# Kernel tuning notes

Measured on AMD Instinct MI355X. Metric: run time of the kernel, lower is better.

Reference implementation:

```python
import jax, jax.numpy as jnp
import numpy as np

NX = 1024
N_HEAD = 16
HEAD_DIM = NX // N_HEAD
MASKED_BIAS = -10000.0


def setup_inputs() -> dict:
    key = jax.random.key(0)
    k1, k2, k3 = jax.random.split(key, 3)
    hidden_states = jax.random.normal(k1, (2, 2048, NX), dtype=jnp.float32)
    # Conv1D weights: stored [in, out], y = x @ W + b (like torch addmm)
    c_attn_w = jax.random.normal(k2, (NX, 3 * NX), dtype=jnp.float32) * 0.02
    c_attn_b = jnp.zeros((3 * NX,), dtype=jnp.float32)
    c_proj_w = jax.random.normal(k3, (NX, NX), dtype=jnp.float32) * 0.02
    c_proj_b = jnp.zeros((NX,), dtype=jnp.float32)
    return {
        "hidden_states": hidden_states,
        "c_attn_w": c_attn_w,
        "c_attn_b": c_attn_b,
        "c_proj_w": c_proj_w,
        "c_proj_b": c_proj_b,
    }


def reference(hidden_states, c_attn_w, c_attn_b, c_proj_w, c_proj_b):
    B, S, _ = hidden_states.shape
    qkv = hidden_states @ c_attn_w + c_attn_b  # [B, S, 3*NX]
    q, k, v = jnp.split(qkv, 3, axis=-1)
    # split heads -> [B, H, S, D]
    def split_heads(x):
        return x.reshape(B, S, N_HEAD, HEAD_DIM).transpose(0, 2, 1, 3)
    q, k, v = split_heads(q), split_heads(k), split_heads(v)
    # scores scaled by sqrt(head_dim) (v.size(-1)**0.5 in original)
    w = jnp.einsum("bhqd,bhkd->bhqk", q, k) / jnp.sqrt(jnp.float32(HEAD_DIM))
    # causal mask (nd == ns here since no past)
    causal = jnp.tril(jnp.ones((S, S), dtype=bool))
    w = jnp.where(causal[None, None, :, :], w, jnp.float32(MASKED_BIAS))
    w = jax.nn.softmax(w, axis=-1)
    a = jnp.einsum("bhqk,bhkd->bhqd", w, v)  # [B, H, S, D]
    # merge heads
    a = a.transpose(0, 2, 1, 3).reshape(B, S, NX)
    out = a @ c_proj_w + c_proj_b
    return out
```

## Files before the change

kernel.cpp:

```cpp
#include <hip/hip_runtime.h>
#include <hip/hip_bf16.h>
#include <cmath>

typedef __attribute__((ext_vector_type(8))) short bf16x8;
typedef __attribute__((ext_vector_type(4))) float f32x4;

#define NXC 1024
#define NH 16
#define HD 64
#define BATCH 2
#define SEQ 2048
#define TOK (BATCH * SEQ)

__device__ __forceinline__ ushort f2bf(float f) {
  unsigned u;
  asm("v_cvt_pk_bf16_f32 %0, %1, %2" : "=v"(u) : "v"(f), "v"(f));
  return (ushort)u;
}

__device__ __forceinline__ void gload_lds16(const void* g, void* lds) {
  __builtin_amdgcn_global_load_lds(
      (const __attribute__((address_space(1))) void*)g,
      (__attribute__((address_space(3))) void*)lds, 16, 0, 0);
}

__device__ __forceinline__ float fast_exp2(float x) {
  float r;
  asm("v_exp_f32 %0, %1" : "=v"(r) : "v"(x));
  return r;
}

template <int CTRL>
__device__ __forceinline__ float dpp_mov(float x) {
  return __builtin_bit_cast(
      float, __builtin_amdgcn_mov_dpp(__builtin_bit_cast(int, x), CTRL, 0xF, 0xF, true));
}
__device__ __forceinline__ float red16_max(float x) {
  x = fmaxf(x, dpp_mov<0x121>(x));
  x = fmaxf(x, dpp_mov<0x122>(x));
  x = fmaxf(x, dpp_mov<0x124>(x));
  x = fmaxf(x, dpp_mov<0x128>(x));
  return x;
}
__device__ __forceinline__ float red16_sum(float x) {
  x += dpp_mov<0x121>(x);
  x += dpp_mov<0x122>(x);
  x += dpp_mov<0x124>(x);
  x += dpp_mov<0x128>(x);
  return x;
}

__global__ __launch_bounds__(256) void k_convert(const float* __restrict__ in,
                                                 ushort* __restrict__ out) {
  int i = (blockIdx.x * 256 + threadIdx.x) * 4;
  float4 v = *(const float4*)(in + i);
  ushort4 o;
  o.x = f2bf(v.x); o.y = f2bf(v.y); o.z = f2bf(v.z); o.w = f2bf(v.w);
  *(ushort4*)(out + i) = o;
}

__global__ __launch_bounds__(256) void k_transpose_w(const float* __restrict__ in,
                                                     ushort* __restrict__ out,
                                                     int Kd, int Nd) {
  __shared__ float t[32][33];
  int n0 = blockIdx.x * 32, k0 = blockIdx.y * 32;
  int tx = threadIdx.x & 31, ty = threadIdx.x >> 5;
#pragma unroll
  for (int r = 0; r < 4; ++r)
    t[tx][ty + r * 8] = in[(size_t)(k0 + ty + r * 8) * Nd + n0 + tx];
  __syncthreads();
  int nl = threadIdx.x >> 3, kq = (threadIdx.x & 7) * 4;
  ushort4 o;
  o.x = f2bf(t[nl][kq + 0]);
  o.y = f2bf(t[nl][kq + 1]);
  o.z = f2bf(t[nl][kq + 2]);
  o.w = f2bf(t[nl][kq + 3]);
  *(ushort4*)&out[(size_t)(n0 + nl) * Kd + k0 + kq] = o;
}

__global__ __launch_bounds__(256) void k_transpose_v(const ushort* __restrict__ in,
                                                     ushort* __restrict__ out) {
  __shared__ ushort t[32][33];
  int bh = blockIdx.z;
  int s0 = blockIdx.x * 32, d0 = blockIdx.y * 32;
  const ushort* ip = in + (size_t)bh * SEQ * HD;
  ushort* op = out + (size_t)bh * HD * SEQ;
  int tx = threadIdx.x & 31, ty = threadIdx.x >> 5;
#pragma unroll
  for (int r = 0; r < 4; ++r)
    t[tx][ty + r * 8] = ip[(size_t)(s0 + ty + r * 8) * HD + d0 + tx];
  __syncthreads();
  int dl = threadIdx.x >> 3, sq = (threadIdx.x & 7) * 4;
  ushort4 o;
  o.x = t[dl][sq + 0]; o.y = t[dl][sq + 1];
  o.z = t[dl][sq + 2]; o.w = t[dl][sq + 3];
  int key = (s0 + sq) ^ ((dl & 7) << 3);
  *(ushort4*)&op[(size_t)(d0 + dl) * SEQ + key] = o;
}

__global__ __launch_bounds__(256) void k_gemm_qkv(const ushort* __restrict__ A,
                                                  const ushort* __restrict__ Bt,
                                                  const float* __restrict__ bias,
                                                  ushort* __restrict__ q_ws,
                                                  ushort* __restrict__ k_ws,
                                                  ushort* __restrict__ v_tmp) {
  __shared__ ushort As[128 * 64];
  __shared__ ushort Bs[128 * 64];
  const int tid = threadIdx.x;
  const int wave = tid >> 6, lane = tid & 63;
  const int xcd = blockIdx.x & 7, loc = blockIdx.x >> 3;
  const int m0 = ((xcd >> 1) * 8 + (loc & 7)) * 128;
  const int n0 = ((xcd & 1) * 12 + (loc >> 3)) * 128;
  const int wr = (wave >> 1) * 64, wc = (wave & 1) * 64;
  const int l15 = lane & 15, lg = lane >> 4;
  f32x4 acc[4][4] = {};
  for (int k0 = 0; k0 < 1024; k0 += 64) {
#pragma unroll
    for (int c = 0; c < 4; ++c) {
      int offB = wave * 4096 + c * 1024 + lane * 16;
      int row = offB >> 7, colB = offB & 127;
      gload_lds16((const char*)A + (size_t)(m0 + row) * 2048 + k0 * 2 + colB,
                  (char*)As + wave * 4096 + c * 1024);
      gload_lds16((const char*)Bt + (size_t)(n0 + row) * 2048 + k0 * 2 + colB,
                  (char*)Bs + wave * 4096 + c * 1024);
    }
    __syncthreads();
#pragma unroll
    for (int kc = 0; kc < 2; ++kc) {
      bf16x8 af[4], bfr[4];
#pragma unroll
      for (int i = 0; i < 4; ++i)
        af[i] = *(const bf16x8*)&As[(wr + i * 16 + l15) * 64 + kc * 32 + lg * 8];
#pragma unroll
      for (int j = 0; j < 4; ++j)
        bfr[j] = *(const bf16x8*)&Bs[(wc + j * 16 + l15) * 64 + kc * 32 + lg * 8];
#pragma unroll
      for (int i = 0; i < 4; ++i)
#pragma unroll
        for (int j = 0; j < 4; ++j)
          acc[i][j] = __builtin_amdgcn_mfma_f32_16x16x32_bf16(af[i], bfr[j], acc[i][j], 0, 0, 0);
    }
    __syncthreads();
  }
#pragma unroll
  for (int j = 0; j < 4; ++j) {
    int col = n0 + wc + j * 16 + l15;
    float bv = bias[col];
    int sec = col >> 10;
    int within = col & 1023;
    int head = within >> 6, d = within & 63;
#pragma unroll
    for (int i = 0; i < 4; ++i) {
#pragma unroll
      for (int r = 0; r < 4; ++r) {
        int row = m0 + wr + i * 16 + lg * 4 + r;
        int b = row >> 11, s = row & 2047;
        float val = acc[i][j][r] + bv;
        size_t hb = ((size_t)(b * NH + head) * SEQ + s) * HD;
        if (sec == 0)      q_ws[hb + d] = f2bf(val * 0.1803368801f);
        else if (sec == 1) k_ws[hb + (d ^ ((s & 7) << 3))] = f2bf(val);
        else               v_tmp[hb + d] = f2bf(val);
      }
    }
  }
}

__global__ __launch_bounds__(256) void k_attn(const ushort* __restrict__ q_ws,
                                              const ushort* __restrict__ k_ws,
                                              const ushort* __restrict__ v_ws,
                                              ushort* __restrict__ a_ws) {
  __shared__ ushort Ks[2][64 * 64];
  __shared__ ushort Vs[2][64 * 64];
  __shared__ ushort Ps[4][2][16 * 64];
  const int p = blockIdx.x, bh = blockIdx.y;
  const int qtA = 31 - p, qtB = p;
  const int tid = threadIdx.x, wave = tid >> 6, lane = tid & 63;
  const int l15 = lane & 15, lg = lane >> 4;
  const int swz = (l15 & 7) << 3;
  const ushort* qp = q_ws + (size_t)bh * SEQ * HD;
  const ushort* kp = k_ws + (size_t)bh * SEQ * HD;
  const ushort* vp = v_ws + (size_t)bh * HD * SEQ;

  bf16x8 qfA[2], qfB[2];
  {
    int qrA = qtA * 64 + wave * 16 + l15;
    int qrB = qtB * 64 + wave * 16 + l15;
    qfA[0] = *(const bf16x8*)&qp[(size_t)qrA * HD + lg * 8];
    qfA[1] = *(const bf16x8*)&qp[(size_t)qrA * HD + 32 + lg * 8];
    qfB[0] = *(const bf16x8*)&qp[(size_t)qrB * HD + lg * 8];
    qfB[1] = *(const bf16x8*)&qp[(size_t)qrB * HD + 32 + lg * 8];
  }
  f32x4 oA[4] = {}, oB[4] = {};
  float mA[4] = {-INFINITY, -INFINITY, -INFINITY, -INFINITY};
  float mB[4] = {-INFINITY, -INFINITY, -INFINITY, -INFINITY};
  float lA[4] = {0.f, 0.f, 0.f, 0.f}, lB[4] = {0.f, 0.f, 0.f, 0.f};

  auto stage = [&](int kt, int buf) {
#pragma unroll
    for (int c = 0; c < 2; ++c) {
      int offB = wave * 2048 + c * 1024 + lane * 16;
      gload_lds16((const char*)kp + (size_t)kt * 8192 + offB,
                  (char*)Ks[buf] + offB);
      int d = offB >> 7, keyB = offB & 127;
      gload_lds16((const char*)vp + (size_t)d * (SEQ * 2) + (size_t)kt * 128 + keyB,
                  (char*)Vs[buf] + offB);
    }
  };

  auto tile_step = [&](const bf16x8* qf, f32x4* o, float* m_r, float* l_r,
                       ushort* Pw, const ushort* Kc, const ushort* Vc, bool diag) {
    f32x4 sc[4] = {};
#pragma unroll
    for (int kc = 0; kc < 2; ++kc)
#pragma unroll
      for (int f = 0; f < 4; ++f) {
        if (diag && f > wave) continue;
        bf16x8 kf = *(const bf16x8*)&Kc[(f * 16 + l15) * 64 + ((kc * 32 + lg * 8) ^ swz)];
        sc[f] = __builtin_amdgcn_mfma_f32_16x16x32_bf16(qf[kc], kf, sc[f], 0, 0, 0);
      }
    if (diag) {
#pragma unroll
      for (int f = 0; f < 4; ++f) {
        int key_rel = f * 16 + l15;
#pragma unroll
        for (int r = 0; r < 4; ++r) {
          int q_rel = wave * 16 + lg * 4 + r;
          if (key_rel > q_rel) sc[f][r] = -1e30f;
        }
      }
    }
    float pm[4];
#pragma unroll
    for (int r = 0; r < 4; ++r)
      pm[r] = fmaxf(fmaxf(sc[0][r], sc[1][r]), fmaxf(sc[2][r], sc[3][r]));
    bool need = false;
#pragma unroll
    for (int r = 0; r < 4; ++r) need |= (pm[r] > m_r[r] + 8.f);
    if (__any(need)) {
#pragma unroll
      for (int r = 0; r < 4; ++r) {
        float full = red16_max(pm[r]);
        float mn = fmaxf(m_r[r], full);
        float al = fast_exp2(m_r[r] - mn);
        m_r[r] = mn;
        l_r[r] *= al;
#pragma unroll
        for (int df = 0; df < 4; ++df) o[df][r] *= al;
      }
    }
#pragma unroll
    for (int f = 0; f < 4; ++f)
#pragma unroll
      for (int r = 0; r < 4; ++r) {
        float pv = fast_exp2(sc[f][r] - m_r[r]);
        l_r[r] += pv;
        int q = lg * 4 + r;
        Pw[q * 64 + ((f * 16 + l15) ^ ((q & 7) << 3))] = f2bf(pv);
      }
#pragma unroll
    for (int kc = 0; kc < 2; ++kc) {
      bf16x8 pf = *(const bf16x8*)&Pw[l15 * 64 + ((kc * 32 + lg * 8) ^ swz)];
#pragma unroll
      for (int df = 0; df < 4; ++df) {
        bf16x8 vf = *(const bf16x8*)&Vc[(df * 16 + l15) * 64 + ((kc * 32 + lg * 8) ^ swz)];
        o[df] = __builtin_amdgcn_mfma_f32_16x16x32_bf16(pf, vf, o[df], 0, 0, 0);
      }
    }
  };

  stage(0, 0);
  asm volatile("s_waitcnt vmcnt(0)" ::: "memory");
  __syncthreads();

  for (int kt = 0; kt <= qtA; ++kt) {
    const int cur = kt & 1;
    if (kt < qtA) stage(kt + 1, cur ^ 1);
    tile_step(qfA, oA, mA, lA, Ps[wave][0], Ks[cur], Vs[cur], kt == qtA);
    if (kt <= qtB)
      tile_step(qfB, oB, mB, lB, Ps[wave][1], Ks[cur], Vs[cur], kt == qtB);
    asm volatile("s_waitcnt vmcnt(0)" ::: "memory");
    __syncthreads();
  }

  int b = bh >> 4, head = bh & 15;
  auto epilogue = [&](f32x4* o, float* l_r, int qt) {
#pragma unroll
    for (int r = 0; r < 4; ++r) {
      float inv = 1.0f / red16_sum(l_r[r]);
      int s = qt * 64 + wave * 16 + lg * 4 + r;
#pragma unroll
      for (int df = 0; df < 4; ++df) {
        int col = head * 64 + df * 16 + l15;
        a_ws[((size_t)(b * SEQ + s)) * NXC + col] = f2bf(o[df][r] * inv);
      }
    }
  };
  epilogue(oA, lA, qtA);
  epilogue(oB, lB, qtB);
}

__global__ __launch_bounds__(256) void k_gemm_proj(const ushort* __restrict__ A,
                                                   const ushort* __restrict__ Bt,
                                                   const float* __restrict__ bias,
                                                   float* __restrict__ out) {
  __shared__ ushort As[128 * 64];
  __shared__ ushort Bs[128 * 64];
  const int tid = threadIdx.x;
  const int wave = tid >> 6, lane = tid & 63;
  const int xcd = blockIdx.x & 7, loc = blockIdx.x >> 3;
  const int m0 = ((xcd >> 1) * 8 + (loc & 7)) * 128;
  const int n0 = ((xcd & 1) * 4 + (loc >> 3)) * 128;
  const int wr = (wave >> 1) * 64, wc = (wave & 1) * 64;
  const int l15 = lane & 15, lg = lane >> 4;
  f32x4 acc[4][4] = {};
  for (int k0 = 0; k0 < 1024; k0 += 64) {
#pragma unroll
    for (int c = 0; c < 4; ++c) {
      int offB = wave * 4096 + c * 1024 + lane * 16;
      int row = offB >> 7, colB = offB & 127;
      gload_lds16((const char*)A + (size_t)(m0 + row) * 2048 + k0 * 2 + colB,
                  (char*)As + wave * 4096 + c * 1024);
      gload_lds16((const char*)Bt + (size_t)(n0 + row) * 2048 + k0 * 2 + colB,
                  (char*)Bs + wave * 4096 + c * 1024);
    }
    __syncthreads();
#pragma unroll
    for (int kc = 0; kc < 2; ++kc) {
      bf16x8 af[4], bfr[4];
#pragma unroll
      for (int i = 0; i < 4; ++i)
        af[i] = *(const bf16x8*)&As[(wr + i * 16 + l15) * 64 + kc * 32 + lg * 8];
#pragma unroll
      for (int j = 0; j < 4; ++j)
        bfr[j] = *(const bf16x8*)&Bs[(wc + j * 16 + l15) * 64 + kc * 32 + lg * 8];
#pragma unroll
      for (int i = 0; i < 4; ++i)
#pragma unroll
        for (int j = 0; j < 4; ++j)
          acc[i][j] = __builtin_amdgcn_mfma_f32_16x16x32_bf16(af[i], bfr[j], acc[i][j], 0, 0, 0);
    }
    __syncthreads();
  }
#pragma unroll
  for (int j = 0; j < 4; ++j) {
    int col = n0 + wc + j * 16 + l15;
    float bv = bias[col];
#pragma unroll
    for (int i = 0; i < 4; ++i) {
#pragma unroll
      for (int r = 0; r < 4; ++r) {
        int row = m0 + wr + i * 16 + lg * 4 + r;
        out[(size_t)row * NXC + col] = acc[i][j][r] + bv;
      }
    }
  }
}

extern "C" void kernel_launch(void* const* d_in, const int* in_sizes, int n_in,
                              void* d_out, int out_size, void* d_ws, size_t ws_size,
                              hipStream_t stream) {
  const float* hs       = (const float*)d_in[0];
  const float* c_attn_w = (const float*)d_in[1];
  const float* c_attn_b = (const float*)d_in[2];
  const float* c_proj_w = (const float*)d_in[3];
  const float* c_proj_b = (const float*)d_in[4];
  char* ws = (char*)d_ws;
  const size_t MB = 1 << 20;
  ushort* Xb      = (ushort*)(ws + 0 * MB);
  ushort* Wt_attn = (ushort*)(ws + 8 * MB);
  ushort* Wt_proj = (ushort*)(ws + 14 * MB);
  ushort* q_ws    = (ushort*)(ws + 16 * MB);
  ushort* k_ws    = (ushort*)(ws + 24 * MB);
  ushort* v_ws    = (ushort*)(ws + 32 * MB);
  ushort* a_ws    = (ushort*)(ws + 40 * MB);
  ushort* v_tmp   = a_ws;

  k_convert<<<4096, 256, 0, stream>>>(hs, Xb);
  k_transpose_w<<<dim3(96, 32), 256, 0, stream>>>(c_attn_w, Wt_attn, 1024, 3072);
  k_transpose_w<<<dim3(32, 32), 256, 0, stream>>>(c_proj_w, Wt_proj, 1024, 1024);
  k_gemm_qkv<<<768, 256, 0, stream>>>(Xb, Wt_attn, c_attn_b, q_ws, k_ws, v_tmp);
  k_transpose_v<<<dim3(64, 2, 32), 256, 0, stream>>>(v_tmp, v_ws);
  k_attn<<<dim3(16, 32), 256, 0, stream>>>(q_ws, k_ws, v_ws, a_ws);
  k_gemm_proj<<<256, 256, 0, stream>>>(a_ws, Wt_proj, c_proj_b, (float*)d_out);
}
```

Measured before the change: 151.1 us.

## Double-buffer GEMM LDS tiles and pre-swizzle operands to avoid bank conflicts

Both the QKV and projection GEMMs now double-buffer their LDS tiles, so global-to-LDS loads for the next K step are issued while the current step runs its MFMAs. All GEMM operands (converted activations, transposed weights, and the attention output) are written to global memory with an XOR swizzle within each 64-element block. The LDS reads apply the same swizzle, which is meant to remove bank conflicts on the bf16x8 fragment loads. This doubles LDS use per block to 64 KB, which may lower occupancy, and it ties the layout conventions of the producer kernels to the GEMM readers.

```diff
diff --git a/kernel.cpp b/kernel.cpp
--- a/kernel.cpp
+++ b/kernel.cpp
@@ -56,7 +56,9 @@
   float4 v = *(const float4*)(in + i);
   ushort4 o;
   o.x = f2bf(v.x); o.y = f2bf(v.y); o.z = f2bf(v.z); o.w = f2bf(v.w);
-  *(ushort4*)(out + i) = o;
+  int row = i >> 10;
+  int dst = (i & ~63) | ((i & 63) ^ ((row & 7) << 3));
+  *(ushort4*)(out + dst) = o;
 }
 
 __global__ __launch_bounds__(256) void k_transpose_w(const float* __restrict__ in,
@@ -75,7 +77,9 @@
   o.y = f2bf(t[nl][kq + 1]);
   o.z = f2bf(t[nl][kq + 2]);
   o.w = f2bf(t[nl][kq + 3]);
-  *(ushort4*)&out[(size_t)(n0 + nl) * Kd + k0 + kq] = o;
+  int row = n0 + nl, kk = k0 + kq;
+  size_t dst = (size_t)row * Kd + (kk & ~63) + ((kk & 63) ^ ((row & 7) << 3));
+  *(ushort4*)&out[dst] = o;
 }
 
 __global__ __launch_bounds__(256) void k_transpose_v(const ushort* __restrict__ in,
@@ -104,8 +108,8 @@
                                                   ushort* __restrict__ q_ws,
                                                   ushort* __restrict__ k_ws,
                                                   ushort* __restrict__ v_tmp) {
-  __shared__ ushort As[128 * 64];
-  __shared__ ushort Bs[128 * 64];
+  __shared__ ushort As[2][128 * 64];
+  __shared__ ushort Bs[2][128 * 64];
   const int tid = threadIdx.x;
   const int wave = tid >> 6, lane = tid & 63;
   const int xcd = blockIdx.x & 7, loc = blockIdx.x >> 3;
@@ -113,33 +117,44 @@
   const int n0 = ((xcd & 1) * 12 + (loc >> 3)) * 128;
   const int wr = (wave >> 1) * 64, wc = (wave & 1) * 64;
   const int l15 = lane & 15, lg = lane >> 4;
+  const int swz = (l15 & 7) << 3;
   f32x4 acc[4][4] = {};
-  for (int k0 = 0; k0 < 1024; k0 += 64) {
+
+  auto stage = [&](int k0, int buf) {
 #pragma unroll
     for (int c = 0; c < 4; ++c) {
       int offB = wave * 4096 + c * 1024 + lane * 16;
       int row = offB >> 7, colB = offB & 127;
       gload_lds16((const char*)A + (size_t)(m0 + row) * 2048 + k0 * 2 + colB,
-                  (char*)As + wave * 4096 + c * 1024);
+                  (char*)As[buf] + wave * 4096 + c * 1024);
       gload_lds16((const char*)Bt + (size_t)(n0 + row) * 2048 + k0 * 2 + colB,
-                  (char*)Bs + wave * 4096 + c * 1024);
-    }
-    __syncthreads();
+                  (char*)Bs[buf] + wave * 4096 + c * 1024);
+    }
+  };
+
+  stage(0, 0);
+  asm volatile("s_waitcnt vmcnt(0)" ::: "memory");
+  __syncthreads();
+
+  for (int kt = 0; kt < 16; ++kt) {
+    const int cur = kt & 1;
+    if (kt < 15) stage((kt + 1) * 64, cur ^ 1);
 #pragma unroll
     for (int kc = 0; kc < 2; ++kc) {
       bf16x8 af[4], bfr[4];
 #pragma unroll
       for (int i = 0; i < 4; ++i)
-        af[i] = *(const bf16x8*)&As[(wr + i * 16 + l15) * 64 + kc * 32 + lg * 8];
+        af[i] = *(const bf16x8*)&As[cur][(wr + i * 16 + l15) * 64 + ((kc * 32 + lg * 8) ^ swz)];
 #pragma unroll
       for (int j = 0; j < 4; ++j)
-        bfr[j] = *(const bf16x8*)&Bs[(wc + j * 16 + l15) * 64 + kc * 32 + lg * 8];
+        bfr[j] = *(const bf16x8*)&Bs[cur][(wc + j * 16 + l15) * 64 + ((kc * 32 + lg * 8) ^ swz)];
 #pragma unroll
       for (int i = 0; i < 4; ++i)
 #pragma unroll
         for (int j = 0; j < 4; ++j)
           acc[i][j] = __builtin_amdgcn_mfma_f32_16x16x32_bf16(af[i], bfr[j], acc[i][j], 0, 0, 0);
     }
+    asm volatile("s_waitcnt vmcnt(0)" ::: "memory");
     __syncthreads();
   }
 #pragma unroll
@@ -290,7 +305,7 @@
       int s = qt * 64 + wave * 16 + lg * 4 + r;
 #pragma unroll
       for (int df = 0; df < 4; ++df) {
-        int col = head * 64 + df * 16 + l15;
+        int col = head * 64 + ((df * 16 + l15) ^ ((s & 7) << 3));
         a_ws[((size_t)(b * SEQ + s)) * NXC + col] = f2bf(o[df][r] * inv);
       }
     }
@@ -303,8 +318,8 @@
                                                    const ushort* __restrict__ Bt,
                                                    const float* __restrict__ bias,
                                                    float* __restrict__ out) {
-  __shared__ ushort As[128 * 64];
-  __shared__ ushort Bs[128 * 64];
+  __shared__ ushort As[2][128 * 64];
+  __shared__ ushort Bs[2][128 * 64];
   const int tid = threadIdx.x;
   const int wave = tid >> 6, lane = tid & 63;
   const int xcd = blockIdx.x & 7, loc = blockIdx.x >> 3;
@@ -312,33 +327,44 @@
   const int n0 = ((xcd & 1) * 4 + (loc >> 3)) * 128;
   const int wr = (wave >> 1) * 64, wc = (wave & 1) * 64;
   const int l15 = lane & 15, lg = lane >> 4;
+  const int swz = (l15 & 7) << 3;
   f32x4 acc[4][4] = {};
-  for (int k0 = 0; k0 < 1024; k0 += 64) {
+
+  auto stage = [&](int k0, int buf) {
 #pragma unroll
     for (int c = 0; c < 4; ++c) {
       int offB = wave * 4096 + c * 1024 + lane * 16;
       int row = offB >> 7, colB = offB & 127;
       gload_lds16((const char*)A + (size_t)(m0 + row) * 2048 + k0 * 2 + colB,
-                  (char*)As + wave * 4096 + c * 1024);
+                  (char*)As[buf] + wave * 4096 + c * 1024);
       gload_lds16((const char*)Bt + (size_t)(n0 + row) * 2048 + k0 * 2 + colB,
-                  (char*)Bs + wave * 4096 + c * 1024);
-    }
-    __syncthreads();
+                  (char*)Bs[buf] + wave * 4096 + c * 1024);
+    }
+  };
+
+  stage(0, 0);
+  asm volatile("s_waitcnt vmcnt(0)" ::: "memory");
+  __syncthreads();
+
+  for (int kt = 0; kt < 16; ++kt) {
+    const int cur = kt & 1;
+    if (kt < 15) stage((kt + 1) * 64, cur ^ 1);
 #pragma unroll
     for (int kc = 0; kc < 2; ++kc) {
       bf16x8 af[4], bfr[4];
 #pragma unroll
       for (int i = 0; i < 4; ++i)
-        af[i] = *(const bf16x8*)&As[(wr + i * 16 + l15) * 64 + kc * 32 + lg * 8];
+        af[i] = *(const bf16x8*)&As[cur][(wr + i * 16 + l15) * 64 + ((kc * 32 + lg * 8) ^ swz)];
 #pragma unroll
       for (int j = 0; j < 4; ++j)
-        bfr[j] = *(const bf16x8*)&Bs[(wc + j * 16 + l15) * 64 + kc * 32 + lg * 8];
+        bfr[j] = *(const bf16x8*)&Bs[cur][(wc + j * 16 + l15) * 64 + ((kc * 32 + lg * 8) ^ swz)];
 #pragma unroll
       for (int i = 0; i < 4; ++i)
 #pragma unroll
         for (int j = 0; j < 4; ++j)
           acc[i][j] = __builtin_amdgcn_mfma_f32_16x16x32_bf16(af[i], bfr[j], acc[i][j], 0, 0, 0);
     }
+    asm volatile("s_waitcnt vmcnt(0)" ::: "memory");
     __syncthreads();
   }
 #pragma unroll
```

Measured after the change: 139.5 us. 7.7% less time.
